# Kernel optimization log

Measured on AMD Instinct MI355X. Metric: run time of the kernel, lower is better.

The kernel has to match this reference:

```python
import jax, jax.numpy as jnp
import numpy as np

N_NODES = 50000
N_EDGES = 1600000
F_IN = 512      # 2 * embedding_dimension
HID = 512
OUT = 4
NEG_SLOPE = 0.01  # torch LeakyReLU default


def _leaky_relu(x):
    return jnp.where(x >= 0, x, NEG_SLOPE * x)


def setup_inputs() -> dict:
    key = jax.random.key(0)
    ks = jax.random.split(key, 12)
    s_in = 1.0 / np.sqrt(F_IN)
    s_h = 1.0 / np.sqrt(HID)
    return {
        "feature": jax.random.normal(ks[0], (N_NODES, F_IN), jnp.float32),
        "edge_index": jax.random.randint(ks[1], (2, N_EDGES), 0, N_NODES, jnp.int64),
        "edge_type": jax.random.randint(ks[2], (N_EDGES,), 0, 2, jnp.int64),
        # input MLP
        "W_in": jax.random.uniform(ks[3], (F_IN, HID), jnp.float32, -s_in, s_in),
        "b_in": jnp.zeros((HID,), jnp.float32),
        # sage1: lin_l (bias) on aggregated neighbors, lin_r (no bias) on self
        "W1_l": jax.random.uniform(ks[4], (HID, HID), jnp.float32, -s_h, s_h),
        "b1_l": jnp.zeros((HID,), jnp.float32),
        "W1_r": jax.random.uniform(ks[5], (HID, HID), jnp.float32, -s_h, s_h),
        # sage2
        "W2_l": jax.random.uniform(ks[6], (HID, HID), jnp.float32, -s_h, s_h),
        "b2_l": jnp.zeros((HID,), jnp.float32),
        "W2_r": jax.random.uniform(ks[7], (HID, HID), jnp.float32, -s_h, s_h),
        # output linear (hidden -> 4); note forward skips linear_relu_output1
        "W_out": jax.random.uniform(ks[8], (HID, OUT), jnp.float32, -s_h, s_h),
        "b_out": jnp.zeros((OUT,), jnp.float32),
    }


def _sage_conv(x, src, dst, W_l, b_l, W_r):
    # mean aggregation of source features onto destinations (PyG default flow)
    agg = jax.ops.segment_sum(x[src], dst, num_segments=N_NODES)  # [N, H]
    cnt = jax.ops.segment_sum(jnp.ones((src.shape[0], 1), x.dtype), dst,
                              num_segments=N_NODES)               # [N, 1]
    mean = agg / jnp.maximum(cnt, 1.0)
    return mean @ W_l + b_l + x @ W_r


def reference(feature, edge_index, edge_type,
              W_in, b_in, W1_l, b1_l, W1_r, W2_l, b2_l, W2_r, W_out, b_out):
    src, dst = edge_index[0], edge_index[1]
    x = _leaky_relu(feature.astype(jnp.float32) @ W_in + b_in)
    x = _sage_conv(x, src, dst, W1_l, b1_l, W1_r)
    # dropout is identity in eval mode
    x = _sage_conv(x, src, dst, W2_l, b2_l, W2_r)
    return x @ W_out + b_out
```

## Files before the change

### kernel.cpp

```cpp
#include <hip/hip_runtime.h>
#include <stdint.h>

#define NNODES 50000
#define NEDGES 1600000
#define HID 512
#define NEG_SLOPE 0.01f
#define NBUCK 98
#define NBLK 200
#define TILE 8000
#define NSUB 8
#define GPBLK 391
#define MROWS 50048

typedef __attribute__((ext_vector_type(8))) short bf16x8;
typedef __attribute__((ext_vector_type(8))) unsigned short u16x8;
typedef __attribute__((ext_vector_type(4))) float f32x4;

__device__ __forceinline__ float bf2f(unsigned short u) {
  unsigned int x = ((unsigned int)u) << 16;
  return __builtin_bit_cast(float, x);
}
__device__ __forceinline__ unsigned short f2bf(float f) {
  unsigned int u = __builtin_bit_cast(unsigned int, f);
  u += 0x7FFFu + ((u >> 16) & 1u);
  return (unsigned short)(u >> 16);
}
__device__ __forceinline__ void gload_lds16(const void* g, void* l) {
  __builtin_amdgcn_global_load_lds(
      (const __attribute__((address_space(1))) void*)g,
      (__attribute__((address_space(3))) void*)l, 16, 0, 0);
}

__global__ void flagk(const int* __restrict__ ei, int* __restrict__ flag) {
  int t = threadIdx.x;
  unsigned long long m = __ballot(ei[2 * t + 1] != 0);
  if (t == 0) *flag = (m != 0ULL) ? 1 : 0;
}

__global__ __launch_bounds__(256) void histk(const int* __restrict__ ei,
                                             const int* __restrict__ flag,
                                             int* __restrict__ hist) {
  __shared__ int h[NBUCK];
  int t = threadIdx.x, blk = blockIdx.x;
  for (int i = t; i < NBUCK; i += 256) h[i] = 0;
  __syncthreads();
  int f = *flag;
  int e0 = blk * TILE;
  for (int e = e0 + 2 * t; e < e0 + TILE; e += 512) {
    int d0, d1;
    if (f) {
      int2 v = *reinterpret_cast<const int2*>(&ei[(size_t)NEDGES + e]);
      d0 = v.x; d1 = v.y;
    } else {
      int4 v = *reinterpret_cast<const int4*>(&ei[2 * ((size_t)NEDGES + e)]);
      d0 = v.x; d1 = v.z;
    }
    if ((unsigned)d0 < NNODES) atomicAdd(&h[d0 >> 9], 1);
    if ((unsigned)d1 < NNODES) atomicAdd(&h[d1 >> 9], 1);
  }
  __syncthreads();
  for (int i = t; i < NBUCK; i += 256) hist[i * NBLK + blk] = h[i];
}

__global__ __launch_bounds__(512) void scanh(int* __restrict__ hist,
                                             int* __restrict__ bstart) {
  __shared__ int s[512];
  const int TOT = NBUCK * NBLK;
  const int C = 40;
  int t = threadIdx.x;
  int base = t * C;
  int sum = 0;
#pragma unroll
  for (int i = 0; i < C; i++) {
    int idx = base + i;
    sum += (idx < TOT) ? hist[idx] : 0;
  }
  s[t] = sum;
  __syncthreads();
  for (int off = 1; off < 512; off <<= 1) {
    int u = (t >= off) ? s[t - off] : 0;
    __syncthreads();
    s[t] += u;
    __syncthreads();
  }
  int run = (t > 0) ? s[t - 1] : 0;
#pragma unroll
  for (int i = 0; i < C; i++) {
    int idx = base + i;
    if (idx < TOT) {
      int v = hist[idx];
      hist[idx] = run;
      if (idx % NBLK == 0) bstart[idx / NBLK] = run;
      run += v;
    }
  }
  if (t == 511) bstart[NBUCK] = s[511];
}

__global__ __launch_bounds__(256) void binscatter(const int* __restrict__ ei,
                                                  const int* __restrict__ flag,
                                                  const int* __restrict__ hbase,
                                                  unsigned int* __restrict__ pcol) {
  __shared__ int lb[NBUCK];
  int t = threadIdx.x, blk = blockIdx.x;
  for (int i = t; i < NBUCK; i += 256) lb[i] = hbase[i * NBLK + blk];
  __syncthreads();
  int f = *flag;
  int e0 = blk * TILE;
  for (int e = e0 + 2 * t; e < e0 + TILE; e += 512) {
    int s0, s1, d0, d1;
    if (f) {
      int2 vs = *reinterpret_cast<const int2*>(&ei[e]);
      int2 vd = *reinterpret_cast<const int2*>(&ei[(size_t)NEDGES + e]);
      s0 = vs.x; s1 = vs.y; d0 = vd.x; d1 = vd.y;
    } else {
      int4 vs = *reinterpret_cast<const int4*>(&ei[2 * (size_t)e]);
      int4 vd = *reinterpret_cast<const int4*>(&ei[2 * ((size_t)NEDGES + e)]);
      s0 = vs.x; s1 = vs.z; d0 = vd.x; d1 = vd.z;
    }
    if ((unsigned)d0 < NNODES) {
      if ((unsigned)s0 >= NNODES) s0 = 0;
      int pos = atomicAdd(&lb[d0 >> 9], 1);
      pcol[pos] = ((unsigned)(d0 & 511) << 16) | (unsigned)s0;
    }
    if ((unsigned)d1 < NNODES) {
      if ((unsigned)s1 >= NNODES) s1 = 0;
      int pos = atomicAdd(&lb[d1 >> 9], 1);
      pcol[pos] = ((unsigned)(d1 & 511) << 16) | (unsigned)s1;
    }
  }
}

__global__ __launch_bounds__(256) void castA(const float* __restrict__ f,
                                             unsigned short* __restrict__ o) {
  int idx = blockIdx.x * 256 + threadIdx.x;
  if (idx >= MROWS * 64) return;
  size_t g = (size_t)idx * 8;
  int row = idx >> 6;
  u16x8 pk;
  if (row < NNODES) {
    float4 v0 = *reinterpret_cast<const float4*>(f + g);
    float4 v1 = *reinterpret_cast<const float4*>(f + g + 4);
    pk[0] = f2bf(v0.x); pk[1] = f2bf(v0.y); pk[2] = f2bf(v0.z); pk[3] = f2bf(v0.w);
    pk[4] = f2bf(v1.x); pk[5] = f2bf(v1.y); pk[6] = f2bf(v1.z); pk[7] = f2bf(v1.w);
  } else {
    pk = (u16x8)0;
  }
  *reinterpret_cast<u16x8*>(o + g) = pk;
}

__global__ void tcast(const float* __restrict__ w, unsigned short* __restrict__ wt) {
  int i = blockIdx.x * 256 + threadIdx.x;
  int n = i >> 9, k = i & 511;
  wt[i] = f2bf(w[(k << 9) | n]);
}

__device__ __forceinline__ float wave_dot(const float* __restrict__ Arow,
                                          const float* __restrict__ B, int j) {
  int l = threadIdx.x & 63;
  float4 a0 = *reinterpret_cast<const float4*>(Arow + l * 8);
  float4 a1 = *reinterpret_cast<const float4*>(Arow + l * 8 + 4);
  const float* bb = B + (size_t)(l * 8) * 4 + j;
  float s = a0.x * bb[0] + a0.y * bb[4] + a0.z * bb[8] + a0.w * bb[12] +
            a1.x * bb[16] + a1.y * bb[20] + a1.z * bb[24] + a1.w * bb[28];
#pragma unroll
  for (int off = 1; off < 64; off <<= 1) s += __shfl_xor(s, off);
  return s;
}

__global__ __launch_bounds__(256) void smallA(
    const float* __restrict__ W2l, const float* __restrict__ W2r,
    const float* __restrict__ Wout, const float* __restrict__ b2l,
    const float* __restrict__ bout,
    float* __restrict__ Wlp, float* __restrict__ Wrp, float* __restrict__ bp) {
  int gw = blockIdx.x * 4 + (threadIdx.x >> 6);
  int l = threadIdx.x & 63;
  if (gw < 2048) {
    float v = wave_dot(W2l + (size_t)(gw >> 2) * 512, Wout, gw & 3);
    if (l == 0) Wlp[gw] = v;
  } else if (gw < 4096) {
    int g = gw - 2048;
    float v = wave_dot(W2r + (size_t)(g >> 2) * 512, Wout, g & 3);
    if (l == 0) Wrp[g] = v;
  } else if (gw < 4100) {
    int j = gw - 4096;
    float v = wave_dot(b2l, Wout, j);
    if (l == 0) bp[j] = v + bout[j];
  }
}

__global__ __launch_bounds__(256) void smallB(
    const float* __restrict__ W1l, const float* __restrict__ W1r,
    const float* __restrict__ b1l,
    const float* __restrict__ Wlp, const float* __restrict__ Wrp,
    const float* __restrict__ bp,
    float* __restrict__ Pall, float* __restrict__ kb, float* __restrict__ kc) {
  int gw = blockIdx.x * 4 + (threadIdx.x >> 6);
  int l = threadIdx.x & 63;
  if (gw < 6144) {
    int k = gw / 12, jg = gw % 12;
    int g = jg >> 2, j = jg & 3;
    float v;
    if (g == 0) v = wave_dot(W1l + (size_t)k * 512, Wlp, j);
    else if (g == 1) v = wave_dot(W1r + (size_t)k * 512, Wlp, j) +
                         wave_dot(W1l + (size_t)k * 512, Wrp, j);
    else v = wave_dot(W1r + (size_t)k * 512, Wrp, j);
    if (l == 0) Pall[k * 12 + jg] = v;
  } else if (gw < 6152) {
    int i = gw - 6144, j = i & 3;
    if (i < 4) {
      float v = wave_dot(b1l, Wlp, j);
      if (l == 0) kb[j] = v;
    } else {
      float v = wave_dot(b1l, Wrp, j);
      if (l == 0) kc[j] = v + bp[j];
    }
  }
}

__global__ __launch_bounds__(256, 4) void gemmproj(
    const unsigned short* __restrict__ Ab, const unsigned short* __restrict__ Bt,
    const float* __restrict__ bias, const float* __restrict__ Pall,
    float* __restrict__ t0p) {
  __shared__ unsigned short As[128 * 32];
  __shared__ unsigned short Bs[128 * 32];
  __shared__ float tab[128 * 12];
  const int tid = threadIdx.x;
  const int wave = tid >> 6, lane = tid & 63;
  const int w = blockIdx.x;
  const int mt = (w & 7) + ((w >> 5) << 3);
  const int nb = (w >> 3) & 3;
  if (mt >= GPBLK) return;
  const int bm = mt * 128, bn = nb * 128;
  const int wr = wave >> 1, wc = wave & 1;
  const int r15 = lane & 15, kl = lane >> 4;
  const int srow = lane >> 2, soff = (lane & 3) * 8;

  for (int i = tid; i < 1536; i += 256) tab[i] = 0.f;

  f32x4 acc[4][4];
#pragma unroll
  for (int i = 0; i < 4; i++)
#pragma unroll
    for (int j = 0; j < 4; j++) acc[i][j] = {0.f, 0.f, 0.f, 0.f};

  for (int kt = 0; kt < HID / 32; ++kt) {
#pragma unroll
    for (int rr = 0; rr < 2; ++rr) {
      int c = wave * 2 + rr;
      int row = c * 16 + srow;
      gload_lds16(Ab + (size_t)(bm + row) * HID + kt * 32 + soff, (void*)&As[c * 512]);
      gload_lds16(Bt + (size_t)(bn + row) * HID + kt * 32 + soff, (void*)&Bs[c * 512]);
    }
    __syncthreads();
    bf16x8 af[4], bfr[4];
#pragma unroll
    for (int mi = 0; mi < 4; ++mi)
      af[mi] = *reinterpret_cast<const bf16x8*>(&As[(wr * 64 + mi * 16 + r15) * 32 + kl * 8]);
#pragma unroll
    for (int ni = 0; ni < 4; ++ni)
      bfr[ni] = *reinterpret_cast<const bf16x8*>(&Bs[(wc * 64 + ni * 16 + r15) * 32 + kl * 8]);
#pragma unroll
    for (int ni = 0; ni < 4; ++ni)
#pragma unroll
      for (int mi = 0; mi < 4; ++mi)
        acc[ni][mi] = __builtin_amdgcn_mfma_f32_16x16x32_bf16(bfr[ni], af[mi], acc[ni][mi], 0, 0, 0);
    __syncthreads();
  }

#pragma unroll
  for (int mi = 0; mi < 4; ++mi) {
    float p12[12];
#pragma unroll
    for (int j = 0; j < 12; ++j) p12[j] = 0.f;
#pragma unroll
    for (int ni = 0; ni < 4; ++ni) {
      int nbase = bn + wc * 64 + ni * 16 + kl * 4;
      float4 bv4 = *reinterpret_cast<const float4*>(bias + nbase);
      float bb[4] = {bv4.x, bv4.y, bv4.z, bv4.w};
#pragma unroll
      for (int rg = 0; rg < 4; ++rg) {
        float v = acc[ni][mi][rg] + bb[rg];
        v = (v >= 0.f) ? v : NEG_SLOPE * v;
        const float* Pc = Pall + (size_t)(nbase + rg) * 12;
        float4 p0 = *reinterpret_cast<const float4*>(Pc);
        float4 p1 = *reinterpret_cast<const float4*>(Pc + 4);
        float4 p2 = *reinterpret_cast<const float4*>(Pc + 8);
        p12[0] += v * p0.x; p12[1] += v * p0.y; p12[2] += v * p0.z; p12[3] += v * p0.w;
        p12[4] += v * p1.x; p12[5] += v * p1.y; p12[6] += v * p1.z; p12[7] += v * p1.w;
        p12[8] += v * p2.x; p12[9] += v * p2.y; p12[10] += v * p2.z; p12[11] += v * p2.w;
      }
    }
#pragma unroll
    for (int j = 0; j < 12; ++j) {
      p12[j] += __shfl_xor(p12[j], 16);
      p12[j] += __shfl_xor(p12[j], 32);
    }
    if (kl == 0) {
      int r = wr * 64 + mi * 16 + r15;
#pragma unroll
      for (int j = 0; j < 12; ++j) atomicAdd(&tab[r * 12 + j], p12[j]);
    }
  }
  __syncthreads();
  float* o = t0p + (size_t)nb * MROWS * 12 + (size_t)bm * 12;
  for (int i = tid; i < 1536; i += 256) o[i] = tab[i];
}

__global__ __launch_bounds__(256) void reduce_t0(const float* __restrict__ t0p,
                                                 float* __restrict__ t0) {
  int i = blockIdx.x * 256 + threadIdx.x;
  if (i >= NNODES * 12) return;
  const size_t S = (size_t)MROWS * 12;
  t0[i] = t0p[i] + t0p[S + i] + t0p[2 * S + i] + t0p[3 * S + i];
}

__global__ __launch_bounds__(256) void aggA(
    const unsigned int* __restrict__ pcol, const int* __restrict__ bstart,
    const float* __restrict__ t0, float* __restrict__ partial) {
  __shared__ float tab[512 * 5];
  int t = threadIdx.x;
  int b = blockIdx.x >> 3, sb = blockIdx.x & 7;
  for (int i = t; i < 2560; i += 256) tab[i] = 0.f;
  __syncthreads();
  int st = bstart[b], en = bstart[b + 1];
  int len = en - st;
  int a0 = st + (int)(((long long)len * sb) >> 3);
  int a1 = st + (int)(((long long)len * (sb + 1)) >> 3);
  for (int e = a0 + t; e < a1; e += 256) {
    unsigned v = pcol[e];
    int i = v >> 16, src = v & 0xFFFF;
    float4 x = *reinterpret_cast<const float4*>(t0 + (size_t)src * 12);
    atomicAdd(&tab[i * 5 + 0], x.x);
    atomicAdd(&tab[i * 5 + 1], x.y);
    atomicAdd(&tab[i * 5 + 2], x.z);
    atomicAdd(&tab[i * 5 + 3], x.w);
    atomicAdd(&tab[i * 5 + 4], 1.f);
  }
  __syncthreads();
  float* o = partial + (size_t)blockIdx.x * 2560;
  for (int i = t; i < 2560; i += 256) o[i] = tab[i];
}

__global__ __launch_bounds__(256) void finA(
    const float* __restrict__ partial, const float* __restrict__ t0,
    float* __restrict__ s1, float* __restrict__ degf) {
  int n = blockIdx.x * 256 + threadIdx.x;
  if (n >= NNODES) return;
  int b = n >> 9, i = n & 511;
  float a[5] = {0.f, 0.f, 0.f, 0.f, 0.f};
#pragma unroll
  for (int s = 0; s < 8; s++) {
    const float* p = partial + (size_t)(b * 8 + s) * 2560 + i * 5;
#pragma unroll
    for (int j = 0; j < 5; j++) a[j] += p[j];
  }
  float deg = a[4];
  float sc = (deg > 0.f) ? 1.f / deg : 0.f;
  float4 tb = *reinterpret_cast<const float4*>(t0 + (size_t)n * 12 + 4);
  float4 o = {a[0] * sc + tb.x, a[1] * sc + tb.y, a[2] * sc + tb.z, a[3] * sc + tb.w};
  *reinterpret_cast<float4*>(s1 + (size_t)n * 4) = o;
  degf[n] = deg;
}

__global__ __launch_bounds__(256) void aggB(
    const unsigned int* __restrict__ pcol, const int* __restrict__ bstart,
    const float* __restrict__ s1, float* __restrict__ partial) {
  __shared__ float tab[512 * 4];
  int t = threadIdx.x;
  int b = blockIdx.x >> 3, sb = blockIdx.x & 7;
  for (int i = t; i < 2048; i += 256) tab[i] = 0.f;
  __syncthreads();
  int st = bstart[b], en = bstart[b + 1];
  int len = en - st;
  int a0 = st + (int)(((long long)len * sb) >> 3);
  int a1 = st + (int)(((long long)len * (sb + 1)) >> 3);
  for (int e = a0 + t; e < a1; e += 256) {
    unsigned v = pcol[e];
    int i = v >> 16, src = v & 0xFFFF;
    float4 x = *reinterpret_cast<const float4*>(s1 + (size_t)src * 4);
    atomicAdd(&tab[i * 4 + 0], x.x);
    atomicAdd(&tab[i * 4 + 1], x.y);
    atomicAdd(&tab[i * 4 + 2], x.z);
    atomicAdd(&tab[i * 4 + 3], x.w);
  }
  __syncthreads();
  float* o = partial + (size_t)blockIdx.x * 2048;
  for (int i = t; i < 2048; i += 256) o[i] = tab[i];
}

__global__ __launch_bounds__(256) void finB(
    const float* __restrict__ partial, const float* __restrict__ t0,
    const float* __restrict__ degf, const float* __restrict__ kb,
    const float* __restrict__ kc, float* __restrict__ out) {
  int n = blockIdx.x * 256 + threadIdx.x;
  if (n >= NNODES) return;
  int b = n >> 9, i = n & 511;
  float a[4] = {0.f, 0.f, 0.f, 0.f};
#pragma unroll
  for (int s = 0; s < 8; s++) {
    const float* p = partial + (size_t)(b * 8 + s) * 2048 + i * 4;
#pragma unroll
    for (int j = 0; j < 4; j++) a[j] += p[j];
  }
  float deg = degf[n];
  float sc = (deg > 0.f) ? 1.f / deg : 0.f;
  float ind = (deg > 0.f) ? 1.f : 0.f;
  float4 c = *reinterpret_cast<const float4*>(t0 + (size_t)n * 12 + 8);
  float4 vb = *reinterpret_cast<const float4*>(kb);
  float4 vc = *reinterpret_cast<const float4*>(kc);
  float4 o = {a[0] * sc + c.x + ind * vb.x + vc.x,
              a[1] * sc + c.y + ind * vb.y + vc.y,
              a[2] * sc + c.z + ind * vb.z + vc.z,
              a[3] * sc + c.w + ind * vb.w + vc.w};
  *reinterpret_cast<float4*>(out + (size_t)n * 4) = o;
}

extern "C" void kernel_launch(void* const* d_in, const int* in_sizes, int n_in,
                              void* d_out, int out_size, void* d_ws, size_t ws_size,
                              hipStream_t stream) {
  const float* feat = (const float*)d_in[0];
  const int* ei = (const int*)d_in[1];
  const float* W_in = (const float*)d_in[3];
  const float* b_in = (const float*)d_in[4];
  const float* W1l = (const float*)d_in[5];
  const float* b1l = (const float*)d_in[6];
  const float* W1r = (const float*)d_in[7];
  const float* W2l = (const float*)d_in[8];
  const float* b2l = (const float*)d_in[9];
  const float* W2r = (const float*)d_in[10];
  const float* Wout = (const float*)d_in[11];
  const float* bout = (const float*)d_in[12];
  float* out = (float*)d_out;

  char* ws = (char*)d_ws;
  size_t off = 0;
  auto alloc = [&](size_t bytes) {
    void* p = ws + off;
    off += (bytes + 15) & ~(size_t)15;
    return p;
  };
  int* flag   = (int*)alloc(16);
  int* hist   = (int*)alloc((size_t)NBUCK * NBLK * 4);
  int* bstart = (int*)alloc((NBUCK + 1) * 4);
  unsigned int* pcol = (unsigned int*)alloc((size_t)NEDGES * 4);
  unsigned short* featb = (unsigned short*)alloc((size_t)MROWS * HID * 2);
  unsigned short* Wt0 = (unsigned short*)alloc(512 * 512 * 2);
  float* Wlp  = (float*)alloc(2048 * 4);
  float* Wrp  = (float*)alloc(2048 * 4);
  float* bp   = (float*)alloc(16);
  float* Pall = (float*)alloc(512 * 12 * 4);
  float* kb   = (float*)alloc(16);
  float* kc   = (float*)alloc(16);
  float* t0   = (float*)alloc((size_t)NNODES * 12 * 4);
  float* t0p  = (float*)alloc((size_t)4 * MROWS * 12 * 4);
  float* s1   = (float*)alloc((size_t)NNODES * 4 * 4);
  float* degf = (float*)alloc((size_t)NNODES * 4);
  float* partial = (float*)alloc((size_t)NBUCK * NSUB * 2560 * 4);
  (void)ws_size;

  flagk<<<1, 64, 0, stream>>>(ei, flag);
  histk<<<NBLK, 256, 0, stream>>>(ei, flag, hist);
  scanh<<<1, 512, 0, stream>>>(hist, bstart);
  binscatter<<<NBLK, 256, 0, stream>>>(ei, flag, hist, pcol);

  castA<<<(MROWS * 64 + 255) / 256, 256, 0, stream>>>(feat, featb);
  tcast<<<1024, 256, 0, stream>>>(W_in, Wt0);
  smallA<<<1025, 256, 0, stream>>>(W2l, W2r, Wout, b2l, bout, Wlp, Wrp, bp);
  smallB<<<1538, 256, 0, stream>>>(W1l, W1r, b1l, Wlp, Wrp, bp, Pall, kb, kc);

  gemmproj<<<1568, 256, 0, stream>>>(featb, Wt0, b_in, Pall, t0p);
  reduce_t0<<<(NNODES * 12 + 255) / 256, 256, 0, stream>>>(t0p, t0);
  aggA<<<NBUCK * NSUB, 256, 0, stream>>>(pcol, bstart, t0, partial);
  finA<<<(NNODES + 255) / 256, 256, 0, stream>>>(partial, t0, s1, degf);
  aggB<<<NBUCK * NSUB, 256, 0, stream>>>(pcol, bstart, s1, partial);
  finB<<<(NNODES + 255) / 256, 256, 0, stream>>>(partial, t0, degf, kb, kc, out);
}
```

Baseline: 303.7 us.

## Fuse prep kernels, double-buffer GEMM, replace partial reductions with atomics

Merges flag detection, weight transpose-cast, feature cast, the small weight products and workspace zeroing into one prep kernel to cut launch count. The projection GEMM gains double-buffered LDS loads so global loads overlap MFMA work. The separate reduce_t0 pass and the per-subblock partial buffers are replaced by global atomicAdds into split t0a/t0b/t0c and per-bucket accumulators, so finA and finB read one value instead of summing eight. This removes extra kernels and memory traffic but adds atomic contention and makes float summation order nondeterministic.

Measured after the change: 289.1 us. -4.8%, faster.

```diff
diff --git a/kernel.cpp b/kernel.cpp
--- a/kernel.cpp
+++ b/kernel.cpp
@@ -12,14 +12,21 @@
 #define GPBLK 391
 #define MROWS 50048
 
+#define ZTOT4 263040
+#define ZBLK 1028
+#define TCBLK 1024
+#define CABLK 12512
+#define SABLK 1025
+#define PREP_TC (ZBLK)
+#define PREP_CA (ZBLK + TCBLK)
+#define PREP_SA (ZBLK + TCBLK + CABLK)
+#define PREP_FLAG (ZBLK + TCBLK + CABLK + SABLK)
+#define PREP_GRID (PREP_FLAG + 1)
+
 typedef __attribute__((ext_vector_type(8))) short bf16x8;
 typedef __attribute__((ext_vector_type(8))) unsigned short u16x8;
 typedef __attribute__((ext_vector_type(4))) float f32x4;
 
-__device__ __forceinline__ float bf2f(unsigned short u) {
-  unsigned int x = ((unsigned int)u) << 16;
-  return __builtin_bit_cast(float, x);
-}
 __device__ __forceinline__ unsigned short f2bf(float f) {
   unsigned int u = __builtin_bit_cast(unsigned int, f);
   u += 0x7FFFu + ((u >> 16) & 1u);
@@ -29,130 +36,6 @@
   __builtin_amdgcn_global_load_lds(
       (const __attribute__((address_space(1))) void*)g,
       (__attribute__((address_space(3))) void*)l, 16, 0, 0);
-}
-
-__global__ void flagk(const int* __restrict__ ei, int* __restrict__ flag) {
-  int t = threadIdx.x;
-  unsigned long long m = __ballot(ei[2 * t + 1] != 0);
-  if (t == 0) *flag = (m != 0ULL) ? 1 : 0;
-}
-
-__global__ __launch_bounds__(256) void histk(const int* __restrict__ ei,
-                                             const int* __restrict__ flag,
-                                             int* __restrict__ hist) {
-  __shared__ int h[NBUCK];
-  int t = threadIdx.x, blk = blockIdx.x;
-  for (int i = t; i < NBUCK; i += 256) h[i] = 0;
-  __syncthreads();
-  int f = *flag;
-  int e0 = blk * TILE;
-  for (int e = e0 + 2 * t; e < e0 + TILE; e += 512) {
-    int d0, d1;
-    if (f) {
-      int2 v = *reinterpret_cast<const int2*>(&ei[(size_t)NEDGES + e]);
-      d0 = v.x; d1 = v.y;
-    } else {
-      int4 v = *reinterpret_cast<const int4*>(&ei[2 * ((size_t)NEDGES + e)]);
-      d0 = v.x; d1 = v.z;
-    }
-    if ((unsigned)d0 < NNODES) atomicAdd(&h[d0 >> 9], 1);
-    if ((unsigned)d1 < NNODES) atomicAdd(&h[d1 >> 9], 1);
-  }
-  __syncthreads();
-  for (int i = t; i < NBUCK; i += 256) hist[i * NBLK + blk] = h[i];
-}
-
-__global__ __launch_bounds__(512) void scanh(int* __restrict__ hist,
-                                             int* __restrict__ bstart) {
-  __shared__ int s[512];
-  const int TOT = NBUCK * NBLK;
-  const int C = 40;
-  int t = threadIdx.x;
-  int base = t * C;
-  int sum = 0;
-#pragma unroll
-  for (int i = 0; i < C; i++) {
-    int idx = base + i;
-    sum += (idx < TOT) ? hist[idx] : 0;
-  }
-  s[t] = sum;
-  __syncthreads();
-  for (int off = 1; off < 512; off <<= 1) {
-    int u = (t >= off) ? s[t - off] : 0;
-    __syncthreads();
-    s[t] += u;
-    __syncthreads();
-  }
-  int run = (t > 0) ? s[t - 1] : 0;
-#pragma unroll
-  for (int i = 0; i < C; i++) {
-    int idx = base + i;
-    if (idx < TOT) {
-      int v = hist[idx];
-      hist[idx] = run;
-      if (idx % NBLK == 0) bstart[idx / NBLK] = run;
-      run += v;
-    }
-  }
-  if (t == 511) bstart[NBUCK] = s[511];
-}
-
-__global__ __launch_bounds__(256) void binscatter(const int* __restrict__ ei,
-                                                  const int* __restrict__ flag,
-                                                  const int* __restrict__ hbase,
-                                                  unsigned int* __restrict__ pcol) {
-  __shared__ int lb[NBUCK];
-  int t = threadIdx.x, blk = blockIdx.x;
-  for (int i = t; i < NBUCK; i += 256) lb[i] = hbase[i * NBLK + blk];
-  __syncthreads();
-  int f = *flag;
-  int e0 = blk * TILE;
-  for (int e = e0 + 2 * t; e < e0 + TILE; e += 512) {
-    int s0, s1, d0, d1;
-    if (f) {
-      int2 vs = *reinterpret_cast<const int2*>(&ei[e]);
-      int2 vd = *reinterpret_cast<const int2*>(&ei[(size_t)NEDGES + e]);
-      s0 = vs.x; s1 = vs.y; d0 = vd.x; d1 = vd.y;
-    } else {
-      int4 vs = *reinterpret_cast<const int4*>(&ei[2 * (size_t)e]);
-      int4 vd = *reinterpret_cast<const int4*>(&ei[2 * ((size_t)NEDGES + e)]);
-      s0 = vs.x; s1 = vs.z; d0 = vd.x; d1 = vd.z;
-    }
-    if ((unsigned)d0 < NNODES) {
-      if ((unsigned)s0 >= NNODES) s0 = 0;
-      int pos = atomicAdd(&lb[d0 >> 9], 1);
-      pcol[pos] = ((unsigned)(d0 & 511) << 16) | (unsigned)s0;
-    }
-    if ((unsigned)d1 < NNODES) {
-      if ((unsigned)s1 >= NNODES) s1 = 0;
-      int pos = atomicAdd(&lb[d1 >> 9], 1);
-      pcol[pos] = ((unsigned)(d1 & 511) << 16) | (unsigned)s1;
-    }
-  }
-}
-
-__global__ __launch_bounds__(256) void castA(const float* __restrict__ f,
-                                             unsigned short* __restrict__ o) {
-  int idx = blockIdx.x * 256 + threadIdx.x;
-  if (idx >= MROWS * 64) return;
-  size_t g = (size_t)idx * 8;
-  int row = idx >> 6;
-  u16x8 pk;
-  if (row < NNODES) {
-    float4 v0 = *reinterpret_cast<const float4*>(f + g);
-    float4 v1 = *reinterpret_cast<const float4*>(f + g + 4);
-    pk[0] = f2bf(v0.x); pk[1] = f2bf(v0.y); pk[2] = f2bf(v0.z); pk[3] = f2bf(v0.w);
-    pk[4] = f2bf(v1.x); pk[5] = f2bf(v1.y); pk[6] = f2bf(v1.z); pk[7] = f2bf(v1.w);
-  } else {
-    pk = (u16x8)0;
-  }
-  *reinterpret_cast<u16x8*>(o + g) = pk;
-}
-
-__global__ void tcast(const float* __restrict__ w, unsigned short* __restrict__ wt) {
-  int i = blockIdx.x * 256 + threadIdx.x;
-  int n = i >> 9, k = i & 511;
-  wt[i] = f2bf(w[(k << 9) | n]);
 }
 
 __device__ __forceinline__ float wave_dot(const float* __restrict__ Arow,
@@ -168,24 +51,57 @@
   return s;
 }
 
-__global__ __launch_bounds__(256) void smallA(
+__global__ __launch_bounds__(256) void prep(
+    const float* __restrict__ feat, const float* __restrict__ W_in,
     const float* __restrict__ W2l, const float* __restrict__ W2r,
     const float* __restrict__ Wout, const float* __restrict__ b2l,
-    const float* __restrict__ bout,
-    float* __restrict__ Wlp, float* __restrict__ Wrp, float* __restrict__ bp) {
-  int gw = blockIdx.x * 4 + (threadIdx.x >> 6);
-  int l = threadIdx.x & 63;
-  if (gw < 2048) {
-    float v = wave_dot(W2l + (size_t)(gw >> 2) * 512, Wout, gw & 3);
-    if (l == 0) Wlp[gw] = v;
-  } else if (gw < 4096) {
-    int g = gw - 2048;
-    float v = wave_dot(W2r + (size_t)(g >> 2) * 512, Wout, g & 3);
-    if (l == 0) Wrp[g] = v;
-  } else if (gw < 4100) {
-    int j = gw - 4096;
-    float v = wave_dot(b2l, Wout, j);
-    if (l == 0) bp[j] = v + bout[j];
+    const float* __restrict__ bout, const int* __restrict__ ei,
+    float* __restrict__ zbase, unsigned short* __restrict__ Wt0,
+    unsigned short* __restrict__ featb,
+    float* __restrict__ Wlp, float* __restrict__ Wrp, float* __restrict__ bp,
+    int* __restrict__ flag) {
+  int blk = blockIdx.x, t = threadIdx.x;
+  if (blk < PREP_TC) {
+    int idx = blk * 256 + t;
+    if (idx < ZTOT4) reinterpret_cast<float4*>(zbase)[idx] = {0.f, 0.f, 0.f, 0.f};
+  } else if (blk < PREP_CA) {
+    int i = (blk - PREP_TC) * 256 + t;
+    int n = i >> 9, k = i & 511;
+    Wt0[i] = f2bf(W_in[(k << 9) | n]);
+  } else if (blk < PREP_SA) {
+    int idx = (blk - PREP_CA) * 256 + t;
+    size_t g = (size_t)idx * 8;
+    int row = idx >> 6;
+    u16x8 pk;
+    if (row < NNODES) {
+      float4 v0 = *reinterpret_cast<const float4*>(feat + g);
+      float4 v1 = *reinterpret_cast<const float4*>(feat + g + 4);
+      pk[0] = f2bf(v0.x); pk[1] = f2bf(v0.y); pk[2] = f2bf(v0.z); pk[3] = f2bf(v0.w);
+      pk[4] = f2bf(v1.x); pk[5] = f2bf(v1.y); pk[6] = f2bf(v1.z); pk[7] = f2bf(v1.w);
+    } else {
+      pk = (u16x8)0;
+    }
+    *reinterpret_cast<u16x8*>(featb + g) = pk;
+  } else if (blk < PREP_FLAG) {
+    int gw = (blk - PREP_SA) * 4 + (t >> 6);
+    int l = t & 63;
+    if (gw < 2048) {
+      float v = wave_dot(W2l + (size_t)(gw >> 2) * 512, Wout, gw & 3);
+      if (l == 0) Wlp[gw] = v;
+    } else if (gw < 4096) {
+      int g = gw - 2048;
+      float v = wave_dot(W2r + (size_t)(g >> 2) * 512, Wout, g & 3);
+      if (l == 0) Wrp[g] = v;
+    } else if (gw < 4100) {
+      int j = gw - 4096;
+      float v = wave_dot(b2l, Wout, j);
+      if (l == 0) bp[j] = v + bout[j];
+    }
+  } else {
+    if (t < 64) {
+      unsigned long long m = __ballot(ei[2 * t + 1] != 0);
+      if (t == 0) *flag = (m != 0ULL) ? 1 : 0;
+    }
   }
 }
 
@@ -218,12 +134,106 @@
   }
 }
 
+__global__ __launch_bounds__(256) void histk(const int* __restrict__ ei,
+                                             const int* __restrict__ flag,
+                                             int* __restrict__ hist) {
+  __shared__ int h[NBUCK];
+  int t = threadIdx.x, blk = blockIdx.x;
+  for (int i = t; i < NBUCK; i += 256) h[i] = 0;
+  __syncthreads();
+  int f = *flag;
+  int e0 = blk * TILE;
+  for (int e = e0 + 2 * t; e < e0 + TILE; e += 512) {
+    int d0, d1;
+    if (f) {
+      int2 v = *reinterpret_cast<const int2*>(&ei[(size_t)NEDGES + e]);
+      d0 = v.x; d1 = v.y;
+    } else {
+      int4 v = *reinterpret_cast<const int4*>(&ei[2 * ((size_t)NEDGES + e)]);
+      d0 = v.x; d1 = v.z;
+    }
+    if ((unsigned)d0 < NNODES) atomicAdd(&h[d0 >> 9], 1);
+    if ((unsigned)d1 < NNODES) atomicAdd(&h[d1 >> 9], 1);
+  }
+  __syncthreads();
+  for (int i = t; i < NBUCK; i += 256) hist[i * NBLK + blk] = h[i];
+}
+
+__global__ __launch_bounds__(512) void scanh(int* __restrict__ hist,
+                                             int* __restrict__ bstart) {
+  __shared__ int s[512];
+  const int TOT = NBUCK * NBLK;
+  const int C = 40;
+  int t = threadIdx.x;
+  int base = t * C;
+  int sum = 0;
+#pragma unroll
+  for (int i = 0; i < C; i++) {
+    int idx = base + i;
+    sum += (idx < TOT) ? hist[idx] : 0;
+  }
+  s[t] = sum;
+  __syncthreads();
+  for (int off = 1; off < 512; off <<= 1) {
+    int u = (t >= off) ? s[t - off] : 0;
+    __syncthreads();
+    s[t] += u;
+    __syncthreads();
+  }
+  int run = (t > 0) ? s[t - 1] : 0;
+#pragma unroll
+  for (int i = 0; i < C; i++) {
+    int idx = base + i;
+    if (idx < TOT) {
+      int v = hist[idx];
+      hist[idx] = run;
+      if (idx % NBLK == 0) bstart[idx / NBLK] = run;
+      run += v;
+    }
+  }
+  if (t == 511) bstart[NBUCK] = s[511];
+}
+
+__global__ __launch_bounds__(256) void binscatter(const int* __restrict__ ei,
+                                                  const int* __restrict__ flag,
+                                                  const int* __restrict__ hbase,
+                                                  unsigned int* __restrict__ pcol) {
+  __shared__ int lb[NBUCK];
+  int t = threadIdx.x, blk = blockIdx.x;
+  for (int i = t; i < NBUCK; i += 256) lb[i] = hbase[i * NBLK + blk];
+  __syncthreads();
+  int f = *flag;
+  int e0 = blk * TILE;
+  for (int e = e0 + 2 * t; e < e0 + TILE; e += 512) {
+    int s0, s1v, d0, d1;
+    if (f) {
+      int2 vs = *reinterpret_cast<const int2*>(&ei[e]);
+      int2 vd = *reinterpret_cast<const int2*>(&ei[(size_t)NEDGES + e]);
+      s0 = vs.x; s1v = vs.y; d0 = vd.x; d1 = vd.y;
+    } else {
+      int4 vs = *reinterpret_cast<const int4*>(&ei[2 * (size_t)e]);
+      int4 vd = *reinterpret_cast<const int4*>(&ei[2 * ((size_t)NEDGES + e)]);
+      s0 = vs.x; s1v = vs.z; d0 = vd.x; d1 = vd.z;
+    }
+    if ((unsigned)d0 < NNODES) {
+      if ((unsigned)s0 >= NNODES) s0 = 0;
+      int pos = atomicAdd(&lb[d0 >> 9], 1);
+      pcol[pos] = ((unsigned)(d0 & 511) << 16) | (unsigned)s0;
+    }
+    if ((unsigned)d1 < NNODES) {
+      if ((unsigned)s1v >= NNODES) s1v = 0;
+      int pos = atomicAdd(&lb[d1 >> 9], 1);
+      pcol[pos] = ((unsigned)(d1 & 511) << 16) | (unsigned)s1v;
+    }
+  }
+}
+
 __global__ __launch_bounds__(256, 4) void gemmproj(
     const unsigned short* __restrict__ Ab, const unsigned short* __restrict__ Bt,
     const float* __restrict__ bias, const float* __restrict__ Pall,
-    float* __restrict__ t0p) {
-  __shared__ unsigned short As[128 * 32];
-  __shared__ unsigned short Bs[128 * 32];
+    float* __restrict__ t0a, float* __restrict__ t0b, float* __restrict__ t0c) {
+  __shared__ unsigned short As[2][128 * 32];
+  __shared__ unsigned short Bs[2][128 * 32];
   __shared__ float tab[128 * 12];
   const int tid = threadIdx.x;
   const int wave = tid >> 6, lane = tid & 63;
@@ -235,6 +245,11 @@
   const int wr = wave >> 1, wc = wave & 1;
   const int r15 = lane & 15, kl = lane >> 4;
   const int srow = lane >> 2, soff = (lane & 3) * 8;
+  const int c0 = wave * 2, c1 = wave * 2 + 1;
+  const unsigned short* ga0 = Ab + (size_t)(bm + c0 * 16 + srow) * HID + soff;
+  const unsigned short* ga1 = Ab + (size_t)(bm + c1 * 16 + srow) * HID + soff;
+  const unsigned short* gb0 = Bt + (size_t)(bn + c0 * 16 + srow) * HID + soff;
+  const unsigned short* gb1 = Bt + (size_t)(bn + c1 * 16 + srow) * HID + soff;
 
   for (int i = tid; i < 1536; i += 256) tab[i] = 0.f;
 
@@ -244,22 +259,29 @@
 #pragma unroll
     for (int j = 0; j < 4; j++) acc[i][j] = {0.f, 0.f, 0.f, 0.f};
 
-  for (int kt = 0; kt < HID / 32; ++kt) {
-#pragma unroll
-    for (int rr = 0; rr < 2; ++rr) {
-      int c = wave * 2 + rr;
-      int row = c * 16 + srow;
-      gload_lds16(Ab + (size_t)(bm + row) * HID + kt * 32 + soff, (void*)&As[c * 512]);
-      gload_lds16(Bt + (size_t)(bn + row) * HID + kt * 32 + soff, (void*)&Bs[c * 512]);
-    }
-    __syncthreads();
+  gload_lds16(ga0, (void*)&As[0][c0 * 512]);
+  gload_lds16(gb0, (void*)&Bs[0][c0 * 512]);
+  gload_lds16(ga1, (void*)&As[0][c1 * 512]);
+  gload_lds16(gb1, (void*)&Bs[0][c1 * 512]);
+  __syncthreads();
+
+  for (int kt = 0; kt < 16; ++kt) {
+    const int cur = kt & 1;
+    if (kt < 15) {
+      const int nxt = cur ^ 1;
+      const int ko = (kt + 1) * 32;
+      gload_lds16(ga0 + ko, (void*)&As[nxt][c0 * 512]);
+      gload_lds16(gb0 + ko, (void*)&Bs[nxt][c0 * 512]);
+      gload_lds16(ga1 + ko, (void*)&As[nxt][c1 * 512]);
+      gload_lds16(gb1 + ko, (void*)&Bs[nxt][c1 * 512]);
+    }
     bf16x8 af[4], bfr[4];
 #pragma unroll
     for (int mi = 0; mi < 4; ++mi)
-      af[mi] = *reinterpret_cast<const bf16x8*>(&As[(wr * 64 + mi * 16 + r15) * 32 + kl * 8]);
+      af[mi] = *reinterpret_cast<const bf16x8*>(&As[cur][(wr * 64 + mi * 16 + r15) * 32 + kl * 8]);
 #pragma unroll
     for (int ni = 0; ni < 4; ++ni)
-      bfr[ni] = *reinterpret_cast<const bf16x8*>(&Bs[(wc * 64 + ni * 16 + r15) * 32 + kl * 8]);
+      bfr[ni] = *reinterpret_cast<const bf16x8*>(&Bs[cur][(wc * 64 + ni * 16 + r15) * 32 + kl * 8]);
 #pragma unroll
     for (int ni = 0; ni < 4; ++ni)
 #pragma unroll
@@ -303,21 +325,19 @@
     }
   }
   __syncthreads();
-  float* o = t0p + (size_t)nb * MROWS * 12 + (size_t)bm * 12;
-  for (int i = tid; i < 1536; i += 256) o[i] = tab[i];
-}
-
-__global__ __launch_bounds__(256) void reduce_t0(const float* __restrict__ t0p,
-                                                 float* __restrict__ t0) {
-  int i = blockIdx.x * 256 + threadIdx.x;
-  if (i >= NNODES * 12) return;
-  const size_t S = (size_t)MROWS * 12;
-  t0[i] = t0p[i] + t0p[S + i] + t0p[2 * S + i] + t0p[3 * S + i];
+  for (int i = tid; i < 1536; i += 256) {
+    int r = i / 12, j = i - r * 12;
+    size_t gr = (size_t)(bm + r);
+    float v = tab[i];
+    if (j < 4) atomicAdd(&t0a[gr * 4 + j], v);
+    else if (j < 8) atomicAdd(&t0b[gr * 4 + (j - 4)], v);
+    else atomicAdd(&t0c[gr * 4 + (j - 8)], v);
+  }
 }
 
 __global__ __launch_bounds__(256) void aggA(
     const unsigned int* __restrict__ pcol, const int* __restrict__ bstart,
-    const float* __restrict__ t0, float* __restrict__ partial) {
+    const float* __restrict__ t0a, float* __restrict__ accA) {
   __shared__ float tab[512 * 5];
   int t = threadIdx.x;
   int b = blockIdx.x >> 3, sb = blockIdx.x & 7;
@@ -330,7 +350,7 @@
   for (int e = a0 + t; e < a1; e += 256) {
     unsigned v = pcol[e];
     int i = v >> 16, src = v & 0xFFFF;
-    float4 x = *reinterpret_cast<const float4*>(t0 + (size_t)src * 12);
+    float4 x = *reinterpret_cast<const float4*>(t0a + (size_t)src * 4);
     atomicAdd(&tab[i * 5 + 0], x.x);
     atomicAdd(&tab[i * 5 + 1], x.y);
     atomicAdd(&tab[i * 5 + 2], x.z);
@@ -338,26 +358,22 @@
     atomicAdd(&tab[i * 5 + 4], 1.f);
   }
   __syncthreads();
-  float* o = partial + (size_t)blockIdx.x * 2560;
-  for (int i = t; i < 2560; i += 256) o[i] = tab[i];
+  float* o = accA + (size_t)b * 2560;
+  for (int i = t; i < 2560; i += 256) {
+    float v = tab[i];
+    if (v != 0.f) atomicAdd(&o[i], v);
+  }
 }
 
 __global__ __launch_bounds__(256) void finA(
-    const float* __restrict__ partial, const float* __restrict__ t0,
+    const float* __restrict__ accA, const float* __restrict__ t0b,
     float* __restrict__ s1, float* __restrict__ degf) {
   int n = blockIdx.x * 256 + threadIdx.x;
   if (n >= NNODES) return;
-  int b = n >> 9, i = n & 511;
-  float a[5] = {0.f, 0.f, 0.f, 0.f, 0.f};
-#pragma unroll
-  for (int s = 0; s < 8; s++) {
-    const float* p = partial + (size_t)(b * 8 + s) * 2560 + i * 5;
-#pragma unroll
-    for (int j = 0; j < 5; j++) a[j] += p[j];
-  }
+  const float* a = accA + (size_t)n * 5;
   float deg = a[4];
   float sc = (deg > 0.f) ? 1.f / deg : 0.f;
-  float4 tb = *reinterpret_cast<const float4*>(t0 + (size_t)n * 12 + 4);
+  float4 tb = *reinterpret_cast<const float4*>(t0b + (size_t)n * 4);
   float4 o = {a[0] * sc + tb.x, a[1] * sc + tb.y, a[2] * sc + tb.z, a[3] * sc + tb.w};
   *reinterpret_cast<float4*>(s1 + (size_t)n * 4) = o;
   degf[n] = deg;
@@ -365,7 +381,7 @@
 
 __global__ __launch_bounds__(256) void aggB(
     const unsigned int* __restrict__ pcol, const int* __restrict__ bstart,
-    const float* __restrict__ s1, float* __restrict__ partial) {
+    const float* __restrict__ s1, float* __restrict__ accB) {
   __shared__ float tab[512 * 4];
   int t = threadIdx.x;
   int b = blockIdx.x >> 3, sb = blockIdx.x & 7;
@@ -385,28 +401,24 @@
     atomicAdd(&tab[i * 4 + 3], x.w);
   }
   __syncthreads();
-  float* o = partial + (size_t)blockIdx.x * 2048;
-  for (int i = t; i < 2048; i += 256) o[i] = tab[i];
+  float* o = accB + (size_t)b * 2048;
+  for (int i = t; i < 2048; i += 256) {
+    float v = tab[i];
+    if (v != 0.f) atomicAdd(&o[i], v);
+  }
 }
 
 __global__ __launch_bounds__(256) void finB(
-    const float* __restrict__ partial, const float* __restrict__ t0,
+    const float* __restrict__ accB, const float* __restrict__ t0c,
     const float* __restrict__ degf, const float* __restrict__ kb,
     const float* __restrict__ kc, float* __restrict__ out) {
   int n = blockIdx.x * 256 + threadIdx.x;
   if (n >= NNODES) return;
-  int b = n >> 9, i = n & 511;
-  float a[4] = {0.f, 0.f, 0.f, 0.f};
-#pragma unroll
-  for (int s = 0; s < 8; s++) {
-    const float* p = partial + (size_t)(b * 8 + s) * 2048 + i * 4;
-#pragma unroll
-    for (int j = 0; j < 4; j++) a[j] += p[j];
-  }
+  const float* a = accB + (size_t)n * 4;
   float deg = degf[n];
   float sc = (deg > 0.f) ? 1.f / deg : 0.f;
   float ind = (deg > 0.f) ? 1.f : 0.f;
-  float4 c = *reinterpret_cast<const float4*>(t0 + (size_t)n * 12 + 8);
+  float4 c = *reinterpret_cast<const float4*>(t0c + (size_t)n * 4);
   float4 vb = *reinterpret_cast<const float4*>(kb);
   float4 vc = *reinterpret_cast<const float4*>(kc);
   float4 o = {a[0] * sc + c.x + ind * vb.x + vc.x,
@@ -440,6 +452,13 @@
     off += (bytes + 15) & ~(size_t)15;
     return p;
   };
+  float* t0a  = (float*)alloc((size_t)MROWS * 4 * 4);
+  float* t0b  = (float*)alloc((size_t)MROWS * 4 * 4);
+  float* t0c  = (float*)alloc((size_t)MROWS * 4 * 4);
+  float* accA = (float*)alloc((size_t)NBUCK * 2560 * 4);
+  float* accB = (float*)alloc((size_t)NBUCK * 2048 * 4);
+  float* zbase = t0a;
+
   int* flag   = (int*)alloc(16);
   int* hist   = (int*)alloc((size_t)NBUCK * NBLK * 4);
   int* bstart = (int*)alloc((NBUCK + 1) * 4);
@@ -452,27 +471,21 @@
   float* Pall = (float*)alloc(512 * 12 * 4);
   float* kb   = (float*)alloc(16);
   float* kc   = (float*)alloc(16);
-  float* t0   = (float*)alloc((size_t)NNODES * 12 * 4);
-  float* t0p  = (float*)alloc((size_t)4 * MROWS * 12 * 4);
-  float* s1   = (float*)alloc((size_t)NNODES * 4 * 4);
+  float* s1   = (float*)alloc((size_t)MROWS * 4 * 4);
   float* degf = (float*)alloc((size_t)NNODES * 4);
-  float* partial = (float*)alloc((size_t)NBUCK * NSUB * 2560 * 4);
   (void)ws_size;
 
-  flagk<<<1, 64, 0, stream>>>(ei, flag);
+  prep<<<PREP_GRID, 256, 0, stream>>>(feat, W_in, W2l, W2r, Wout, b2l, bout, ei,
+                                      zbase, Wt0, featb, Wlp, Wrp, bp, flag);
+  smallB<<<1538, 256, 0, stream>>>(W1l, W1r, b1l, Wlp, Wrp, bp, Pall, kb, kc);
+
   histk<<<NBLK, 256, 0, stream>>>(ei, flag, hist);
   scanh<<<1, 512, 0, stream>>>(hist, bstart);
   binscatter<<<NBLK, 256, 0, stream>>>(ei, flag, hist, pcol);
 
-  castA<<<(MROWS * 64 + 255) / 256, 256, 0, stream>>>(feat, featb);
-  tcast<<<1024, 256, 0, stream>>>(W_in, Wt0);
-  smallA<<<1025, 256, 0, stream>>>(W2l, W2r, Wout, b2l, bout, Wlp, Wrp, bp);
-  smallB<<<1538, 256, 0, stream>>>(W1l, W1r, b1l, Wlp, Wrp, bp, Pall, kb, kc);
-
-  gemmproj<<<1568, 256, 0, stream>>>(featb, Wt0, b_in, Pall, t0p);
-  reduce_t0<<<(NNODES * 12 + 255) / 256, 256, 0, stream>>>(t0p, t0);
-  aggA<<<NBUCK * NSUB, 256, 0, stream>>>(pcol, bstart, t0, partial);
-  finA<<<(NNODES + 255) / 256, 256, 0, stream>>>(partial, t0, s1, degf);
-  aggB<<<NBUCK * NSUB, 256, 0, stream>>>(pcol, bstart, s1, partial);
-  finB<<<(NNODES + 255) / 256, 256, 0, stream>>>(partial, t0, degf, kb, kc, out);
-}
+  gemmproj<<<1568, 256, 0, stream>>>(featb, Wt0, b_in, Pall, t0a, t0b, t0c);
+  aggA<<<NBUCK * NSUB, 256, 0, stream>>>(pcol, bstart, t0a, accA);
+  finA<<<(NNODES + 255) / 256, 256, 0, stream>>>(accA, t0b, s1, degf);
+  aggB<<<NBUCK * NSUB, 256, 0, stream>>>(pcol, bstart, s1, accB);
+  finB<<<(NNODES + 255) / 256, 256, 0, stream>>>(accB, t0c, degf, kb, kc, out);
+}
```
